# Kernel optimization log

Hardware: AMD Instinct MI355X
Metric: run time of the kernel (lower is better)

The kernel has to match this reference:

```python
import math
import jax, jax.numpy as jnp
import numpy as np

N_INPUTS, N_OUTPUTS = 2049, 1024
OUT_START, OUT_END, IN_END = 25.0, 24000.0, 24000.0


def _build_buffers(n_inputs=N_INPUTS, n_outputs=N_OUTPUTS, output_start=OUT_START,
                   output_end=OUT_END, input_end=IN_END):
    # Mirrors LogScale.__init__ (numpy, construction-time, exact).
    scale = 1.0
    min_log = math.log10(1.0 + scale * output_start)
    max_log = math.log10(1.0 + scale * output_end)
    lin_logs = np.linspace(min_log, max_log, n_outputs, dtype=np.float64)
    freq_per_bin = scale * float(input_end) / (n_inputs - 1)
    center_bins = ((np.power(10.0, lin_logs) - 1.0) / freq_per_bin).astype(np.float32)
    n_linear = 0
    while n_linear < n_outputs - 1 and (center_bins[n_linear + 1] - center_bins[n_linear] <= 1.0 or center_bins[n_linear] < 1.0):
        n_linear += 1
    output_start_idx = center_bins[:n_linear].astype(np.int64)
    fraction_linear = center_bins[:n_linear] - output_start_idx.astype(np.float32)
    linear_pair_idx = (np.concatenate([output_start_idx, output_start_idx + 1])
                       if n_linear > 0 else np.zeros(0, dtype=np.int64))
    n_sum = n_linear
    while n_sum < n_outputs - 2 and (center_bins[n_sum + 1] - center_bins[n_sum] <= 2.0 or center_bins[n_sum] < 2.0):
        n_sum += 1
    fraction_cubic = center_bins[n_linear:n_sum].copy()
    n_tri = n_outputs - n_sum
    ft = center_bins[n_sum:n_sum + n_tri]
    dt = center_bins[n_sum:n_sum + n_tri] - center_bins[n_sum - 1:n_sum - 1 + n_tri]
    weights = np.full((max(n_tri, 1), n_inputs), -np.inf, dtype=np.float32)
    for i in range(n_tri):
        i_mid = int(math.ceil(ft[i]))
        i_start = int(math.ceil(ft[i] - dt[i]))
        i_end = int(math.ceil(ft[i] + dt[i + 1])) if i < n_tri - 1 else i_mid
        weights[i, i_mid] = 0.0
        dist_left = float(i_mid - i_start)
        for ib in range(i_start + 1, i_mid):
            weights[i, ib] = np.float32(10.0 * np.log10(1.0 - (i_mid - ib) / dist_left))
        if i_end > i_mid:
            dist_right = float(i_end - i_mid)
            for ib in range(i_mid + 1, i_end):
                weights[i, ib] = np.float32(10.0 * np.log10(np.float32(1.0 - (ib - i_mid) / dist_right)))
    return linear_pair_idx, fraction_linear, fraction_cubic, weights[:n_tri]


def setup_inputs() -> dict:
    key = jax.random.key(0)
    x = jax.random.normal(key, (32, 512, N_INPUTS), dtype=jnp.float32)
    pidx, flin, fcub, w = _build_buffers()
    return {
        "x": x,
        "fraction_linear": jnp.asarray(flin),
        "fraction_cubic": jnp.asarray(fcub),
        "triangular_weights": jnp.asarray(w),
        "linear_pair_idx": jnp.asarray(pidx, dtype=jnp.int32),
    }


_TRI_CHUNK = 128  # rows of flattened x per lax.map step (bounds the dense intermediate)


def _tri_max(flat, w):
    # (x[:, None, :] + w).max(-1), chunked along N to keep the (chunk, n_tri, n_in)
    # intermediate bounded, mirroring the torch _triangular_amax chunking.
    n, n_in = flat.shape
    pad = (-n) % _TRI_CHUNK
    flat_p = jnp.pad(flat, ((0, pad), (0, 0)))
    xb = flat_p.reshape(-1, _TRI_CHUNK, n_in)
    out = jax.lax.map(lambda xc: jnp.max(xc[:, None, :] + w[None, :, :], axis=-1), xb)
    return out.reshape(-1, w.shape[0])[:n]


def _forward(x, fraction_linear, fraction_cubic, triangular_weights, linear_pair_idx):
    lead = x.shape[:-1]
    n_lin = fraction_linear.shape[0]
    outs = []
    if n_lin > 0:
        pair = jnp.take(x, linear_pair_idx, axis=-1).reshape(*lead, 2, n_lin)
        x0, x1 = pair[..., 0, :], pair[..., 1, :]
        outs.append(x0 + fraction_linear * (x1 - x0))
    if fraction_cubic.shape[0] > 0:
        i0 = jnp.floor(fraction_cubic).astype(jnp.int32)
        f = fraction_cubic - i0.astype(fraction_cubic.dtype)
        g = lambda off: jnp.take(x, i0 + off, axis=-1)
        xm1, xc0, xc1, xc2 = g(-1), g(0), g(1), g(2)
        # Catmull-Rom cubic interpolation at fractional position f in [0,1)
        cubic = xc0 + 0.5 * f * ((xc1 - xm1) + f * ((2.0 * xm1 - 5.0 * xc0 + 4.0 * xc1 - xc2)
                                                    + f * (3.0 * (xc0 - xc1) + xc2 - xm1)))
        outs.append(cubic)
    if triangular_weights.shape[0] > 0:
        flat = x.reshape(-1, x.shape[-1])
        outs.append(_tri_max(flat, triangular_weights).reshape(*lead, triangular_weights.shape[0]))
    return jnp.concatenate(outs, axis=-1)


def reference(x, fraction_linear, fraction_cubic, triangular_weights, linear_pair_idx):
    return _forward(x, fraction_linear, fraction_cubic, triangular_weights, linear_pair_idx)
```

## Files before the change

### kernel.cpp

```cpp
#include <hip/hip_runtime.h>
#include <math.h>

#define NI 2049
#define ROWS 4
#define WCAP 4096
#define NTRI_MAX 512

__global__ void logscale_win(const float* __restrict__ w, int n_in,
                             int* __restrict__ tri_start,
                             int* __restrict__ tri_cnt) {
    const int i = blockIdx.x;
    __shared__ int smin, smax;
    if (threadIdx.x == 0) { smin = n_in; smax = -1; }
    __syncthreads();
    int lmin = n_in, lmax = -1;
    const float* wr = w + (size_t)i * n_in;
    for (int b = threadIdx.x; b < n_in; b += blockDim.x) {
        float v = wr[b];
        if (v > -1e30f) { lmin = min(lmin, b); lmax = max(lmax, b); }
    }
    atomicMin(&smin, lmin);
    atomicMax(&smax, lmax);
    __syncthreads();
    if (threadIdx.x == 0) {
        int s = smin, cnt = smax - smin + 1;
        if (cnt < 1) { s = 0; cnt = 1; }
        if (cnt > 64) cnt = 64;
        tri_start[i] = s; tri_cnt[i] = cnt;
    }
}

__global__ void logscale_pack(const float* __restrict__ w,
                              const float* __restrict__ flin,
                              const float* __restrict__ fcub,
                              const int*   __restrict__ pidx,
                              const int*   __restrict__ tri_start,
                              const int*   __restrict__ tri_cnt,
                              float4* __restrict__ meta,
                              float*  __restrict__ wpk,
                              int*    __restrict__ d_total,
                              int n_lin, int n_cub, int n_tri) {
    __shared__ int offs[NTRI_MAX + 1];
    __shared__ int starts[NTRI_MAX];
    const int tid = threadIdx.x;
    for (int i = tid; i < n_tri; i += blockDim.x) {
        offs[i + 1] = tri_cnt[i];
        starts[i]   = tri_start[i];
    }
    if (tid == 0) offs[0] = 0;
    __syncthreads();

    if (tid < 64) {
        int v[8];
        int run = 0;
        const int base = tid * 8;
        #pragma unroll
        for (int k = 0; k < 8; ++k) {
            int idx = base + k;
            int c = (idx < n_tri) ? offs[idx + 1] : 0;
            run += c;
            v[k] = run;
        }
        int tot = run;
        #pragma unroll
        for (int d = 1; d < 64; d <<= 1) {
            int up = __shfl_up(tot, (unsigned)d, 64);
            if (tid >= d) tot += up;
        }
        const int excl = tot - run;
        #pragma unroll
        for (int k = 0; k < 8; ++k) {
            int idx = base + k;
            if (idx < n_tri) offs[idx + 1] = excl + v[k];
        }
    }
    __syncthreads();
    if (tid == 0) {
        int t = offs[n_tri]; if (t > WCAP) t = WCAP;
        *d_total = t;
    }

    const int n_out = n_lin + n_cub + n_tri;
    for (int o = tid; o < n_out; o += blockDim.x) {
        float4 m;
        if (o < n_lin) {
            m.x = __int_as_float(pidx[o]);
            m.y = __int_as_float(pidx[n_lin + o]);
            m.z = flin[o]; m.w = 0.0f;
        } else if (o < n_lin + n_cub) {
            float c = fcub[o - n_lin];
            int i0 = (int)floorf(c);
            m.x = __int_as_float(i0);
            m.y = 0.0f;
            m.z = c - (float)i0; m.w = 0.0f;
        } else {
            int i = o - n_lin - n_cub;
            int oa = min(offs[i], WCAP), ob = min(offs[i + 1], WCAP);
            m.x = __int_as_float(starts[i]);
            m.y = __int_as_float(ob - oa);
            m.z = __int_as_float(oa); m.w = 0.0f;
        }
        meta[o] = m;
    }

    const int wv = tid >> 6, ln = tid & 63;
    for (int i = wv; i < n_tri; i += 4) {
        const int oa = min(offs[i], WCAP);
        const int ob = min(offs[i + 1], WCAP);
        if (ln < ob - oa)
            wpk[oa + ln] = w[(size_t)i * NI + starts[i] + ln];
    }
}

__global__ __launch_bounds__(256) void logscale_main(
    const float*  __restrict__ x,
    const float4* __restrict__ meta,
    const float*  __restrict__ wpk,
    const int*    __restrict__ d_total,
    float* __restrict__ out,
    int n_lin, int n_cub, int n_out, int n_rows) {

    __shared__ __align__(16) float xs[ROWS * NI];
    __shared__ __align__(16) float wl[WCAP];

    const int tid  = threadIdx.x;
    const int row0 = blockIdx.x * ROWS;
    const int rows_here = min(ROWS, n_rows - row0);

    const float* xr = x + (size_t)row0 * NI;
    const int nx = rows_here * NI;
    const int nq = nx >> 2;
    const float4* xr4 = (const float4*)xr;
    float4* xs4 = (float4*)xs;
    for (int i = tid; i < nq; i += 256) xs4[i] = xr4[i];
    for (int i = (nq << 2) + tid; i < nx; i += 256) xs[i] = xr[i];

    const int tw  = *d_total;
    const int twq = (tw + 3) >> 2;
    const float4* wp4 = (const float4*)wpk;
    float4* wl4 = (float4*)wl;
    for (int i = tid; i < twq; i += 256) wl4[i] = wp4[i];
    __syncthreads();

    const int n_lc = n_lin + n_cub;
    float* ob = out + (size_t)row0 * n_out;

    if (rows_here == ROWS) {
        for (int o = tid; o < n_out; o += 256) {
            const float4 m = meta[o];
            float res[ROWS];
            if (o < n_lin) {
                const int i0 = __float_as_int(m.x);
                const int i1 = __float_as_int(m.y);
                const float f = m.z;
                #pragma unroll
                for (int r = 0; r < ROWS; ++r) {
                    const int b = r * NI;
                    const float x0 = xs[b + i0];
                    const float x1 = xs[b + i1];
                    res[r] = x0 + f * (x1 - x0);
                }
            } else if (o < n_lc) {
                const int i0 = __float_as_int(m.x);
                const float f = m.z;
                #pragma unroll
                for (int r = 0; r < ROWS; ++r) {
                    const int b = r * NI + i0;
                    const float xm1 = xs[b - 1];
                    const float x0  = xs[b];
                    const float x1  = xs[b + 1];
                    const float x2  = xs[b + 2];
                    res[r] = x0 + 0.5f * f * (x1 - xm1 +
                             f * (2.0f * xm1 - 5.0f * x0 + 4.0f * x1 - x2 +
                             f * (3.0f * (x0 - x1) + x2 - xm1)));
                }
            } else {
                const int s   = __float_as_int(m.x);
                const int cnt = __float_as_int(m.y);
                const int off = __float_as_int(m.z);
                const float* wj = wl + off;
                const float* xp = xs + s;
                float acc0 = -INFINITY, acc1 = -INFINITY;
                float acc2 = -INFINITY, acc3 = -INFINITY;
                for (int j = 0; j < cnt; ++j) {
                    const float wv = wj[j];
                    acc0 = fmaxf(acc0, xp[j] + wv);
                    acc1 = fmaxf(acc1, xp[j + NI] + wv);
                    acc2 = fmaxf(acc2, xp[j + 2 * NI] + wv);
                    acc3 = fmaxf(acc3, xp[j + 3 * NI] + wv);
                }
                res[0] = acc0; res[1] = acc1; res[2] = acc2; res[3] = acc3;
            }
            #pragma unroll
            for (int r = 0; r < ROWS; ++r)
                ob[(size_t)r * n_out + o] = res[r];
        }
    } else {
        for (int o = tid; o < n_out; o += 256) {
            const float4 m = meta[o];
            for (int r = 0; r < rows_here; ++r) {
                const int b = r * NI;
                float res;
                if (o < n_lin) {
                    const int i0 = __float_as_int(m.x);
                    const int i1 = __float_as_int(m.y);
                    const float f = m.z;
                    const float x0 = xs[b + i0];
                    const float x1 = xs[b + i1];
                    res = x0 + f * (x1 - x0);
                } else if (o < n_lc) {
                    const int i0 = __float_as_int(m.x) + b;
                    const float f = m.z;
                    const float xm1 = xs[i0 - 1];
                    const float x0  = xs[i0];
                    const float x1  = xs[i0 + 1];
                    const float x2  = xs[i0 + 2];
                    res = x0 + 0.5f * f * (x1 - xm1 +
                          f * (2.0f * xm1 - 5.0f * x0 + 4.0f * x1 - x2 +
                          f * (3.0f * (x0 - x1) + x2 - xm1)));
                } else {
                    const int s   = __float_as_int(m.x) + b;
                    const int cnt = __float_as_int(m.y);
                    const int off = __float_as_int(m.z);
                    float mx = -INFINITY;
                    for (int j = 0; j < cnt; ++j)
                        mx = fmaxf(mx, xs[s + j] + wl[off + j]);
                    res = mx;
                }
                ob[(size_t)r * n_out + o] = res;
            }
        }
    }
}

extern "C" void kernel_launch(void* const* d_in, const int* in_sizes, int n_in,
                              void* d_out, int out_size, void* d_ws, size_t ws_size,
                              hipStream_t stream) {
    (void)n_in; (void)ws_size; (void)out_size;
    const float* x    = (const float*)d_in[0];
    const float* flin = (const float*)d_in[1];
    const float* fcub = (const float*)d_in[2];
    const float* w    = (const float*)d_in[3];
    const int*   pidx = (const int*)d_in[4];
    float* out = (float*)d_out;

    const int n_lin  = in_sizes[1];
    const int n_cub  = in_sizes[2];
    const int n_tri  = in_sizes[3] / NI;
    const int n_rows = in_sizes[0] / NI;
    const int n_out  = n_lin + n_cub + n_tri;

    float4* meta      = (float4*)d_ws;
    float*  wpk       = (float*)(meta + n_out);
    int*    tri_start = (int*)(wpk + WCAP);
    int*    tri_cnt   = tri_start + NTRI_MAX;
    int*    d_total   = tri_cnt + NTRI_MAX;

    if (n_tri > 0)
        logscale_win<<<n_tri, 256, 0, stream>>>(w, NI, tri_start, tri_cnt);
    logscale_pack<<<1, 256, 0, stream>>>(w, flin, fcub, pidx, tri_start, tri_cnt,
                                         meta, wpk, d_total, n_lin, n_cub, n_tri);
    const int nblk = (n_rows + ROWS - 1) / ROWS;
    logscale_main<<<nblk, 256, 0, stream>>>(x, meta, wpk, d_total, out,
                                            n_lin, n_cub, n_out, n_rows);
}
```

Baseline: 282.2 us.

## Drop shared-memory staging and tile main kernel over output columns

The main kernel no longer copies each block's four input rows and the packed weights into LDS. Instead it launches one block per (row tile, output tile) pair, and each thread reads x and the weights directly from global memory through the caches. This removes the per-block staging cost and the LDS occupancy limit, and gives more parallelism across output columns. In exchange the gathers become uncoalesced global loads, and the same rows are re-read by each output tile.

```diff
diff --git a/kernel.cpp b/kernel.cpp
--- a/kernel.cpp
+++ b/kernel.cpp
@@ -3,6 +3,7 @@
 
 #define NI 2049
 #define ROWS 4
+#define BT 256
 #define WCAP 4096
 #define NTRI_MAX 512
 
@@ -112,123 +113,103 @@
     }
 }
 
-__global__ __launch_bounds__(256) void logscale_main(
+__global__ __launch_bounds__(BT) void logscale_main(
     const float*  __restrict__ x,
     const float4* __restrict__ meta,
     const float*  __restrict__ wpk,
-    const int*    __restrict__ d_total,
     float* __restrict__ out,
-    int n_lin, int n_cub, int n_out, int n_rows) {
-
-    __shared__ __align__(16) float xs[ROWS * NI];
-    __shared__ __align__(16) float wl[WCAP];
-
-    const int tid  = threadIdx.x;
-    const int row0 = blockIdx.x * ROWS;
+    int n_lin, int n_cub, int n_out, int n_rows, int n_otiles) {
+
+    const int ot   = blockIdx.x % n_otiles;
+    const int rt   = blockIdx.x / n_otiles;
+    const int o    = ot * BT + threadIdx.x;
+    const int row0 = rt * ROWS;
     const int rows_here = min(ROWS, n_rows - row0);
-
+    if (o >= n_out) return;
+
+    const float4 m = meta[o];
+    const int n_lc = n_lin + n_cub;
     const float* xr = x + (size_t)row0 * NI;
-    const int nx = rows_here * NI;
-    const int nq = nx >> 2;
-    const float4* xr4 = (const float4*)xr;
-    float4* xs4 = (float4*)xs;
-    for (int i = tid; i < nq; i += 256) xs4[i] = xr4[i];
-    for (int i = (nq << 2) + tid; i < nx; i += 256) xs[i] = xr[i];
-
-    const int tw  = *d_total;
-    const int twq = (tw + 3) >> 2;
-    const float4* wp4 = (const float4*)wpk;
-    float4* wl4 = (float4*)wl;
-    for (int i = tid; i < twq; i += 256) wl4[i] = wp4[i];
-    __syncthreads();
-
-    const int n_lc = n_lin + n_cub;
-    float* ob = out + (size_t)row0 * n_out;
+    float* ob = out + (size_t)row0 * n_out + o;
 
     if (rows_here == ROWS) {
-        for (int o = tid; o < n_out; o += 256) {
-            const float4 m = meta[o];
-            float res[ROWS];
+        float res[ROWS];
+        if (o < n_lin) {
+            const int i0 = __float_as_int(m.x);
+            const int i1 = __float_as_int(m.y);
+            const float f = m.z;
+            #pragma unroll
+            for (int r = 0; r < ROWS; ++r) {
+                const float x0 = xr[r * NI + i0];
+                const float x1 = xr[r * NI + i1];
+                res[r] = x0 + f * (x1 - x0);
+            }
+        } else if (o < n_lc) {
+            const int i0 = __float_as_int(m.x);
+            const float f = m.z;
+            #pragma unroll
+            for (int r = 0; r < ROWS; ++r) {
+                const float* xp = xr + r * NI + i0;
+                const float xm1 = xp[-1];
+                const float x0  = xp[0];
+                const float x1  = xp[1];
+                const float x2  = xp[2];
+                res[r] = x0 + 0.5f * f * (x1 - xm1 +
+                         f * (2.0f * xm1 - 5.0f * x0 + 4.0f * x1 - x2 +
+                         f * (3.0f * (x0 - x1) + x2 - xm1)));
+            }
+        } else {
+            const int s   = __float_as_int(m.x);
+            const int cnt = __float_as_int(m.y);
+            const int off = __float_as_int(m.z);
+            const float* wj = wpk + off;
+            const float* xp = xr + s;
+            float acc0 = -INFINITY, acc1 = -INFINITY;
+            float acc2 = -INFINITY, acc3 = -INFINITY;
+            #pragma unroll 4
+            for (int j = 0; j < cnt; ++j) {
+                const float wv = wj[j];
+                acc0 = fmaxf(acc0, xp[j] + wv);
+                acc1 = fmaxf(acc1, xp[j + NI] + wv);
+                acc2 = fmaxf(acc2, xp[j + 2 * NI] + wv);
+                acc3 = fmaxf(acc3, xp[j + 3 * NI] + wv);
+            }
+            res[0] = acc0; res[1] = acc1; res[2] = acc2; res[3] = acc3;
+        }
+        #pragma unroll
+        for (int r = 0; r < ROWS; ++r)
+            ob[(size_t)r * n_out] = res[r];
+    } else {
+        for (int r = 0; r < rows_here; ++r) {
+            const float* xrr = xr + r * NI;
+            float res;
             if (o < n_lin) {
                 const int i0 = __float_as_int(m.x);
                 const int i1 = __float_as_int(m.y);
                 const float f = m.z;
-                #pragma unroll
-                for (int r = 0; r < ROWS; ++r) {
-                    const int b = r * NI;
-                    const float x0 = xs[b + i0];
-                    const float x1 = xs[b + i1];
-                    res[r] = x0 + f * (x1 - x0);
-                }
+                const float x0 = xrr[i0];
+                const float x1 = xrr[i1];
+                res = x0 + f * (x1 - x0);
             } else if (o < n_lc) {
                 const int i0 = __float_as_int(m.x);
                 const float f = m.z;
-                #pragma unroll
-                for (int r = 0; r < ROWS; ++r) {
-                    const int b = r * NI + i0;
-                    const float xm1 = xs[b - 1];
-                    const float x0  = xs[b];
-                    const float x1  = xs[b + 1];
-                    const float x2  = xs[b + 2];
-                    res[r] = x0 + 0.5f * f * (x1 - xm1 +
-                             f * (2.0f * xm1 - 5.0f * x0 + 4.0f * x1 - x2 +
-                             f * (3.0f * (x0 - x1) + x2 - xm1)));
-                }
+                const float xm1 = xrr[i0 - 1];
+                const float x0  = xrr[i0];
+                const float x1  = xrr[i0 + 1];
+                const float x2  = xrr[i0 + 2];
+                res = x0 + 0.5f * f * (x1 - xm1 +
+                      f * (2.0f * xm1 - 5.0f * x0 + 4.0f * x1 - x2 +
+                      f * (3.0f * (x0 - x1) + x2 - xm1)));
             } else {
                 const int s   = __float_as_int(m.x);
                 const int cnt = __float_as_int(m.y);
                 const int off = __float_as_int(m.z);
-                const float* wj = wl + off;
-                const float* xp = xs + s;
-                float acc0 = -INFINITY, acc1 = -INFINITY;
-                float acc2 = -INFINITY, acc3 = -INFINITY;
-                for (int j = 0; j < cnt; ++j) {
-                    const float wv = wj[j];
-                    acc0 = fmaxf(acc0, xp[j] + wv);
-                    acc1 = fmaxf(acc1, xp[j + NI] + wv);
-                    acc2 = fmaxf(acc2, xp[j + 2 * NI] + wv);
-                    acc3 = fmaxf(acc3, xp[j + 3 * NI] + wv);
-                }
-                res[0] = acc0; res[1] = acc1; res[2] = acc2; res[3] = acc3;
-            }
-            #pragma unroll
-            for (int r = 0; r < ROWS; ++r)
-                ob[(size_t)r * n_out + o] = res[r];
-        }
-    } else {
-        for (int o = tid; o < n_out; o += 256) {
-            const float4 m = meta[o];
-            for (int r = 0; r < rows_here; ++r) {
-                const int b = r * NI;
-                float res;
-                if (o < n_lin) {
-                    const int i0 = __float_as_int(m.x);
-                    const int i1 = __float_as_int(m.y);
-                    const float f = m.z;
-                    const float x0 = xs[b + i0];
-                    const float x1 = xs[b + i1];
-                    res = x0 + f * (x1 - x0);
-                } else if (o < n_lc) {
-                    const int i0 = __float_as_int(m.x) + b;
-                    const float f = m.z;
-                    const float xm1 = xs[i0 - 1];
-                    const float x0  = xs[i0];
-                    const float x1  = xs[i0 + 1];
-                    const float x2  = xs[i0 + 2];
-                    res = x0 + 0.5f * f * (x1 - xm1 +
-                          f * (2.0f * xm1 - 5.0f * x0 + 4.0f * x1 - x2 +
-                          f * (3.0f * (x0 - x1) + x2 - xm1)));
-                } else {
-                    const int s   = __float_as_int(m.x) + b;
-                    const int cnt = __float_as_int(m.y);
-                    const int off = __float_as_int(m.z);
-                    float mx = -INFINITY;
-                    for (int j = 0; j < cnt; ++j)
-                        mx = fmaxf(mx, xs[s + j] + wl[off + j]);
-                    res = mx;
-                }
-                ob[(size_t)r * n_out + o] = res;
-            }
+                float mx = -INFINITY;
+                for (int j = 0; j < cnt; ++j)
+                    mx = fmaxf(mx, xrr[s + j] + wpk[off + j]);
+                res = mx;
+            }
+            ob[(size_t)r * n_out] = res;
         }
     }
 }
@@ -260,7 +241,8 @@
         logscale_win<<<n_tri, 256, 0, stream>>>(w, NI, tri_start, tri_cnt);
     logscale_pack<<<1, 256, 0, stream>>>(w, flin, fcub, pidx, tri_start, tri_cnt,
                                          meta, wpk, d_total, n_lin, n_cub, n_tri);
-    const int nblk = (n_rows + ROWS - 1) / ROWS;
-    logscale_main<<<nblk, 256, 0, stream>>>(x, meta, wpk, d_total, out,
-                                            n_lin, n_cub, n_out, n_rows);
-}
+    const int n_otiles = (n_out + BT - 1) / BT;
+    const int n_rtiles = (n_rows + ROWS - 1) / ROWS;
+    logscale_main<<<n_rtiles * n_otiles, BT, 0, stream>>>(
+        x, meta, wpk, out, n_lin, n_cub, n_out, n_rows, n_otiles);
+}
```

After: 399.5 us. 41.6% more time.
